# Performance work log

Hardware: AMD Instinct MI355X
Metric: run time of the kernel (lower is better)

The kernel has to match this reference:

```python
import jax, jax.numpy as jnp
import numpy as np

THR = 0.6
EPS = 1e-12


def _mlp(x, w1, b1, w2, b2):
    # Linear -> ReLU -> (Dropout eval = identity) -> Linear
    return jax.nn.relu(x @ w1 + b1) @ w2 + b2


def setup_inputs() -> dict:
    B, H, D = 16384, 1024, 300
    key = jax.random.key(0)
    ks = jax.random.split(key, 32)
    s = 0.02
    inp = {
        'brics': jax.random.normal(ks[0], (B, H), jnp.float32),
        'function_group': jax.random.normal(ks[1], (B, H), jnp.float32),
        'pharmacophore': jax.random.normal(ks[2], (B, H), jnp.float32),
        # fingerprint encoders (brics / function_group / pharmacophore)
        'bw1': jax.random.normal(ks[3], (H, D), jnp.float32) * s,
        'bb1': jnp.zeros((D,), jnp.float32),
        'bw2': jax.random.normal(ks[4], (D, H), jnp.float32) * s,
        'bb2': jnp.zeros((H,), jnp.float32),
        'fw1': jax.random.normal(ks[5], (H, D), jnp.float32) * s,
        'fb1': jnp.zeros((D,), jnp.float32),
        'fw2': jax.random.normal(ks[6], (D, H), jnp.float32) * s,
        'fb2': jnp.zeros((H,), jnp.float32),
        'pw1': jax.random.normal(ks[7], (H, D), jnp.float32) * s,
        'pb1': jnp.zeros((D,), jnp.float32),
        'pw2': jax.random.normal(ks[8], (D, H), jnp.float32) * s,
        'pb2': jnp.zeros((H,), jnp.float32),
        # weight generator: Linear(3H, 3)
        'wg_W': jax.random.normal(ks[9], (3 * H, 3), jnp.float32) * s,
        'wg_b': jnp.zeros((3,), jnp.float32),
        # enhancement layer: Linear(H, H) + sigmoid
        'enh_W': jax.random.normal(ks[10], (H, H), jnp.float32) * s,
        'enh_b': jnp.zeros((H,), jnp.float32),
        # fusion layer: Linear(2H, H)
        'fus_W': jax.random.normal(ks[11], (2 * H, H), jnp.float32) * s,
        'fus_b': jnp.zeros((H,), jnp.float32),
    }
    return inp


def reference(brics, function_group, pharmacophore,
              bw1, bb1, bw2, bb2,
              fw1, fb1, fw2, fb2,
              pw1, pb1, pw2, pb2,
              wg_W, wg_b, enh_W, enh_b, fus_W, fus_b):
    B, H = brics.shape
    eb = _mlp(brics, bw1, bb1, bw2, bb2)            # [B,H]
    ef = _mlp(function_group, fw1, fb1, fw2, fb2)   # [B,H]
    ep = _mlp(pharmacophore, pw1, pb1, pw2, pb2)    # [B,H]

    E = jnp.stack([eb, ef, ep], axis=1)             # [B,3,H]
    En = E / jnp.maximum(jnp.linalg.norm(E, axis=-1, keepdims=True), EPS)

    # three unordered pairs (0,1),(0,2),(1,2); softmax-weighted sum is
    # permutation invariant, so the original python sort is a no-op.
    ii = jnp.array([0, 0, 1])
    jj = jnp.array([1, 2, 2])
    Ei, Ej = E[:, ii], E[:, jj]                     # [B,3,H]
    Eni, Enj = En[:, ii], En[:, jj]
    sim = jnp.sum(Eni * Enj, axis=-1)               # [B,3] cosine sims
    keep = sim > THR                                # pairs above threshold

    elem_mask = (Eni * Enj > THR).astype(E.dtype)   # [B,3,H]
    cf = 0.5 * (Ei + Ej) * elem_mask                # candidate common feats

    w = jax.nn.softmax(jnp.where(keep, sim, -1e9), axis=-1)  # [B,3]
    wsum = jnp.einsum('bp,bph->bh', w, cf)
    mean_fp = jnp.mean(E, axis=1)
    any_kept = jnp.any(keep, axis=-1, keepdims=True)
    common = jnp.where(any_kept, wsum, mean_fp)     # [B,H]

    all_cat = jnp.concatenate([eb, ef, ep], axis=1)          # [B,3H]
    fp_w = jax.nn.softmax(all_cat @ wg_W + wg_b, axis=1)     # [B,3]
    weighted_fp_sum = jnp.einsum('bk,bkh->bh', fp_w, E)

    enh = jax.nn.sigmoid(common @ enh_W + enh_b)
    enhanced_common = common * enh

    fused = jnp.concatenate([weighted_fp_sum, enhanced_common], axis=1) @ fus_W + fus_b
    return fused
```

## Files before the change

kernel.cpp:

```cpp
#include <hip/hip_runtime.h>
#include <stdint.h>


typedef __attribute__((ext_vector_type(8))) __bf16 bf16x8;
typedef __attribute__((ext_vector_type(8))) short short8;
typedef __attribute__((ext_vector_type(4))) float floatx4;

__device__ __forceinline__ uint16_t f2bf(float f) {
  union { float f; uint32_t u; } v; v.f = f;
  uint32_t r = v.u + 0x7fffu + ((v.u >> 16) & 1u);
  return (uint16_t)(r >> 16);
}
__device__ __forceinline__ float bf2f(uint16_t h) {
  union { uint32_t u; float f; } v; v.u = ((uint32_t)h) << 16;
  return v.f;
}
__device__ __forceinline__ void gload16(const void* g, void* l) {
  __builtin_amdgcn_global_load_lds(
      (const __attribute__((address_space(1))) void*)g,
      (__attribute__((address_space(3))) void*)l, 16, 0, 0);
}

__global__ void cfe_cvt3_kernel(const float* __restrict__ s0,
                                const float* __restrict__ s1,
                                const float* __restrict__ s2,
                                uint16_t* __restrict__ dst) {
  const float* s = (blockIdx.y == 0) ? s0 : ((blockIdx.y == 1) ? s1 : s2);
  long i = (long)blockIdx.x * 256 + threadIdx.x;
  float4 v = ((const float4*)s)[i];
  ushort4 o;
  o.x = f2bf(v.x); o.y = f2bf(v.y); o.z = f2bf(v.z); o.w = f2bf(v.w);
  ((ushort4*)dst)[(long)blockIdx.y * (16384L * 1024 / 4) + i] = o;
}

__global__ void cfe_transpose_cvt_kernel(const float* __restrict__ src,
                                         uint16_t* __restrict__ dst,
                                         int K, int N, int Kpad, int Npad) {
  __shared__ float tile[32][33];
  const int tx = threadIdx.x & 31;
  const int ty = threadIdx.x >> 5;
  const int k0 = blockIdx.x * 32;
  const int n0 = blockIdx.y * 32;
#pragma unroll
  for (int i = 0; i < 4; i++) {
    int k = k0 + ty + 8 * i;
    int n = n0 + tx;
    tile[ty + 8 * i][tx] = (k < K && n < N) ? src[(long)k * N + n] : 0.f;
  }
  __syncthreads();
#pragma unroll
  for (int i = 0; i < 4; i++) {
    int n = n0 + ty + 8 * i;
    int k = k0 + tx;
    if (n < Npad && k < Kpad) dst[(long)n * Kpad + k] = f2bf(tile[tx][ty + 8 * i]);
  }
}

template <int MODE>
__global__ void cfe_gemm128(const uint16_t* __restrict__ A, long sAz, int lda,
                            const uint16_t* __restrict__ Bt, long sBz, int ldb,
                            void* __restrict__ C, long sCz, int ldc, int colofs,
                            const float* __restrict__ bias0,
                            const float* __restrict__ bias1,
                            const float* __restrict__ bias2, int biasN,
                            const uint16_t* __restrict__ common, int K) {
  const int z = blockIdx.z;
  A += (long)z * sAz;
  Bt += (long)z * sBz;
  const float* bias = (z == 0) ? bias0 : ((z == 1) ? bias1 : bias2);

  const int tid = threadIdx.x;
  const int wave = tid >> 6;
  const int lane = tid & 63;
  const int wm = wave >> 1;
  const int wn = wave & 1;
  const long bm = (long)blockIdx.y * 128;
  const long bn = (long)blockIdx.x * 128;

  __shared__ __attribute__((aligned(16))) uint16_t As[128 * 32];
  __shared__ __attribute__((aligned(16))) uint16_t Bs[128 * 32];

  floatx4 acc[4][4];
#pragma unroll
  for (int i = 0; i < 4; i++)
#pragma unroll
    for (int j = 0; j < 4; j++) acc[i][j] = (floatx4){0.f, 0.f, 0.f, 0.f};

  const int lrow = lane >> 2;
  const int lcol = (lane & 3) * 8;
  const uint16_t* Ap = A + (bm + wave * 32 + lrow) * (long)lda + lcol;
  const uint16_t* Bp = Bt + (bn + wave * 32 + lrow) * (long)ldb + lcol;
  uint16_t* AsW0 = &As[(wave * 32) * 32];
  uint16_t* AsW1 = &As[(wave * 32 + 16) * 32];
  uint16_t* BsW0 = &Bs[(wave * 32) * 32];
  uint16_t* BsW1 = &Bs[(wave * 32 + 16) * 32];

  const int fr = lane & 15;
  const int fq = lane >> 4;
  const uint16_t* ArBase = &As[(wm * 64 + fr) * 32 + fq * 8];
  const uint16_t* BrBase = &Bs[(wn * 64 + fr) * 32 + fq * 8];

  for (int k0 = 0; k0 < K; k0 += 32) {
    gload16(Ap + k0, AsW0);
    gload16(Ap + 16 * (long)lda + k0, AsW1);
    gload16(Bp + k0, BsW0);
    gload16(Bp + 16 * (long)ldb + k0, BsW1);
    __syncthreads();

    short8 a[4], b[4];
#pragma unroll
    for (int mi = 0; mi < 4; mi++) a[mi] = *(const short8*)(ArBase + mi * 16 * 32);
#pragma unroll
    for (int ni = 0; ni < 4; ni++) b[ni] = *(const short8*)(BrBase + ni * 16 * 32);
#pragma unroll
    for (int mi = 0; mi < 4; mi++)
#pragma unroll
      for (int ni = 0; ni < 4; ni++)
        acc[mi][ni] = __builtin_amdgcn_mfma_f32_16x16x32_bf16(
            __builtin_bit_cast(bf16x8, a[mi]), __builtin_bit_cast(bf16x8, b[ni]),
            acc[mi][ni], 0, 0, 0);
    __syncthreads();
  }

#pragma unroll
  for (int mi = 0; mi < 4; mi++) {
    long row = bm + wm * 64 + mi * 16 + fq * 4;
#pragma unroll
    for (int ni = 0; ni < 4; ni++) {
      long col = bn + wn * 64 + ni * 16 + fr;
      float bv = (col < biasN) ? bias[col] : 0.f;
#pragma unroll
      for (int r = 0; r < 4; r++) {
        float v = acc[mi][ni][r] + bv;
        long idx = (row + r) * (long)ldc + colofs + col;
        if constexpr (MODE == 0) {
          ((uint16_t*)C)[(long)z * sCz + idx] = f2bf(fmaxf(v, 0.f));
        } else if constexpr (MODE == 1) {
          ((uint16_t*)C)[(long)z * sCz + idx] = f2bf(v);
        } else if constexpr (MODE == 2) {
          float c = bf2f(common[(row + r) * 1024 + col]);
          float s = 1.f / (1.f + __expf(-v));
          ((uint16_t*)C)[idx] = f2bf(c * s);
        } else {
          ((float*)C)[idx] = v;
        }
      }
    }
  }
}

__global__ void cfe_pointwise_kernel(const uint16_t* __restrict__ E,
                                     const float* __restrict__ wgW,
                                     const float* __restrict__ wgb,
                                     uint16_t* __restrict__ commonb,
                                     uint16_t* __restrict__ fusedA) {
  const int row = blockIdx.x;
  const int tid = threadIdx.x;
  const long ES = 16384L * 1024;
  const long base = (long)row * 1024 + tid * 4;

  ushort4 u0 = *(const ushort4*)(E + base);
  ushort4 u1 = *(const ushort4*)(E + ES + base);
  ushort4 u2 = *(const ushort4*)(E + 2 * ES + base);
  float eb[4] = {bf2f(u0.x), bf2f(u0.y), bf2f(u0.z), bf2f(u0.w)};
  float ef[4] = {bf2f(u1.x), bf2f(u1.y), bf2f(u1.z), bf2f(u1.w)};
  float ep[4] = {bf2f(u2.x), bf2f(u2.y), bf2f(u2.z), bf2f(u2.w)};

  float vals[9];
#pragma unroll
  for (int i = 0; i < 9; i++) vals[i] = 0.f;
#pragma unroll
  for (int j = 0; j < 4; j++) {
    int h = tid * 4 + j;
    vals[0] += eb[j] * eb[j];
    vals[1] += ef[j] * ef[j];
    vals[2] += ep[j] * ep[j];
    vals[3] += eb[j] * ef[j];
    vals[4] += eb[j] * ep[j];
    vals[5] += ef[j] * ep[j];
#pragma unroll
    for (int c = 0; c < 3; c++)
      vals[6 + c] += eb[j] * wgW[(long)h * 3 + c] +
                     ef[j] * wgW[(long)(1024 + h) * 3 + c] +
                     ep[j] * wgW[(long)(2048 + h) * 3 + c];
  }

#pragma unroll
  for (int i = 0; i < 9; i++) {
    float v = vals[i];
    for (int off = 32; off; off >>= 1) v += __shfl_down(v, off);
    vals[i] = v;
  }
  __shared__ float red[4][9];
  if ((tid & 63) == 0) {
#pragma unroll
    for (int i = 0; i < 9; i++) red[tid >> 6][i] = vals[i];
  }
  __syncthreads();
  float tot[9];
#pragma unroll
  for (int i = 0; i < 9; i++)
    tot[i] = red[0][i] + red[1][i] + red[2][i] + red[3][i];

  const float EPSF = 1e-12f;
  float nb = fmaxf(sqrtf(tot[0]), EPSF);
  float nf = fmaxf(sqrtf(tot[1]), EPSF);
  float np_ = fmaxf(sqrtf(tot[2]), EPSF);
  float s01 = tot[3] / (nb * nf);
  float s02 = tot[4] / (nb * np_);
  float s12 = tot[5] / (nf * np_);
  bool k01 = s01 > 0.6f, k02 = s02 > 0.6f, k12 = s12 > 0.6f;
  bool any = k01 | k02 | k12;
  float z0 = k01 ? s01 : -1e9f;
  float z1 = k02 ? s02 : -1e9f;
  float z2 = k12 ? s12 : -1e9f;
  float zm = fmaxf(z0, fmaxf(z1, z2));
  float w0 = __expf(z0 - zm), w1 = __expf(z1 - zm), w2 = __expf(z2 - zm);
  float wsum = w0 + w1 + w2;
  w0 /= wsum; w1 /= wsum; w2 /= wsum;

  float g0 = tot[6] + wgb[0], g1 = tot[7] + wgb[1], g2 = tot[8] + wgb[2];
  float gm = fmaxf(g0, fmaxf(g1, g2));
  float f0 = __expf(g0 - gm), f1 = __expf(g1 - gm), f2 = __expf(g2 - gm);
  float fs = f0 + f1 + f2;
  f0 /= fs; f1 /= fs; f2 /= fs;

  float inb = 1.f / nb, inf_ = 1.f / nf, inp = 1.f / np_;
  ushort4 co, wf;
  uint16_t cov[4], wfv[4];
#pragma unroll
  for (int j = 0; j < 4; j++) {
    float b = eb[j], f = ef[j], p = ep[j];
    float nbv = b * inb, nfv = f * inf_, npv = p * inp;
    float c01 = (nbv * nfv > 0.6f) ? 0.5f * (b + f) : 0.f;
    float c02 = (nbv * npv > 0.6f) ? 0.5f * (b + p) : 0.f;
    float c12 = (nfv * npv > 0.6f) ? 0.5f * (f + p) : 0.f;
    float ws = w0 * c01 + w1 * c02 + w2 * c12;
    float cm = any ? ws : (b + f + p) * (1.f / 3.f);
    float wfs = f0 * b + f1 * f + f2 * p;
    cov[j] = f2bf(cm);
    wfv[j] = f2bf(wfs);
  }
  co.x = cov[0]; co.y = cov[1]; co.z = cov[2]; co.w = cov[3];
  wf.x = wfv[0]; wf.y = wfv[1]; wf.z = wfv[2]; wf.w = wfv[3];
  *(ushort4*)(commonb + base) = co;
  *(ushort4*)(fusedA + (long)row * 2048 + tid * 4) = wf;
}

extern "C" void kernel_launch(void* const* d_in, const int* in_sizes, int n_in,
                              void* d_out, int out_size, void* d_ws, size_t ws_size,
                              hipStream_t stream) {
  (void)in_sizes; (void)n_in; (void)out_size; (void)ws_size;
  const float* brics = (const float*)d_in[0];
  const float* fg    = (const float*)d_in[1];
  const float* ph    = (const float*)d_in[2];
  const float* bw1 = (const float*)d_in[3];  const float* bb1 = (const float*)d_in[4];
  const float* bw2 = (const float*)d_in[5];  const float* bb2 = (const float*)d_in[6];
  const float* fw1 = (const float*)d_in[7];  const float* fb1 = (const float*)d_in[8];
  const float* fw2 = (const float*)d_in[9];  const float* fb2 = (const float*)d_in[10];
  const float* pw1 = (const float*)d_in[11]; const float* pb1 = (const float*)d_in[12];
  const float* pw2 = (const float*)d_in[13]; const float* pb2 = (const float*)d_in[14];
  const float* wgW = (const float*)d_in[15]; const float* wgb = (const float*)d_in[16];
  const float* enhW = (const float*)d_in[17]; const float* enhb = (const float*)d_in[18];
  const float* fusW = (const float*)d_in[19]; const float* fusb = (const float*)d_in[20];
  float* out = (float*)d_out;

  uint16_t* XB   = (uint16_t*)d_ws;
  uint16_t* EB   = XB;
  uint16_t* FA   = XB + 3L * 16384 * 1024;
  uint16_t* W1T  = FA + 16384L * 2048;
  uint16_t* W2T  = W1T + 3L * 384 * 1024;
  uint16_t* ENHT = W2T + 3L * 1024 * 320;
  uint16_t* FUST = ENHT + 1024L * 1024;
  uint16_t* YB   = (uint16_t*)d_out;
  uint16_t* COM  = (uint16_t*)d_out;

  cfe_cvt3_kernel<<<dim3(16384, 3), 256, 0, stream>>>(brics, fg, ph, XB);

  cfe_transpose_cvt_kernel<<<dim3(32, 12), 256, 0, stream>>>(bw1, W1T + 0L * 384 * 1024, 1024, 300, 1024, 384);
  cfe_transpose_cvt_kernel<<<dim3(32, 12), 256, 0, stream>>>(fw1, W1T + 1L * 384 * 1024, 1024, 300, 1024, 384);
  cfe_transpose_cvt_kernel<<<dim3(32, 12), 256, 0, stream>>>(pw1, W1T + 2L * 384 * 1024, 1024, 300, 1024, 384);
  cfe_transpose_cvt_kernel<<<dim3(10, 32), 256, 0, stream>>>(bw2, W2T + 0L * 1024 * 320, 300, 1024, 320, 1024);
  cfe_transpose_cvt_kernel<<<dim3(10, 32), 256, 0, stream>>>(fw2, W2T + 1L * 1024 * 320, 300, 1024, 320, 1024);
  cfe_transpose_cvt_kernel<<<dim3(10, 32), 256, 0, stream>>>(pw2, W2T + 2L * 1024 * 320, 300, 1024, 320, 1024);
  cfe_transpose_cvt_kernel<<<dim3(32, 32), 256, 0, stream>>>(enhW, ENHT, 1024, 1024, 1024, 1024);
  cfe_transpose_cvt_kernel<<<dim3(64, 32), 256, 0, stream>>>(fusW, FUST, 2048, 1024, 2048, 1024);

  cfe_gemm128<0><<<dim3(3, 128, 3), 256, 0, stream>>>(
      XB, 16384L * 1024, 1024, W1T, 384L * 1024, 1024,
      YB, 16384L * 384, 384, 0, bb1, fb1, pb1, 300, nullptr, 1024);

  cfe_gemm128<1><<<dim3(8, 128, 3), 256, 0, stream>>>(
      YB, 16384L * 384, 384, W2T, 1024L * 320, 320,
      EB, 16384L * 1024, 1024, 0, bb2, fb2, pb2, 1024, nullptr, 320);

  cfe_pointwise_kernel<<<16384, 256, 0, stream>>>(EB, wgW, wgb, COM, FA);

  cfe_gemm128<2><<<dim3(8, 128, 1), 256, 0, stream>>>(
      COM, 0, 1024, ENHT, 0, 1024,
      FA, 0, 2048, 1024, enhb, enhb, enhb, 1024, COM, 1024);

  cfe_gemm128<3><<<dim3(8, 128, 1), 256, 0, stream>>>(
      FA, 0, 2048, FUST, 0, 2048,
      out, 0, 1024, 0, fusb, fusb, fusb, 1024, nullptr, 2048);
}
```

Measured before the change: 625.8 us.

## Fuse fp32-to-bf16 input conversion into first GEMM and remap block order

Removes the separate conversion kernel that turned the three fp32 input matrices into bf16. The first GEMM now reads fp32 directly, converts to bf16 in registers and stores into LDS, which avoids writing and re-reading a 96MB intermediate. Block indices are remapped with an 8-way interleave, meant to improve cache locality across concurrently running blocks. The eight weight-transpose launches are merged into four batched launches. The trade-off is that A loads in the first GEMM become synchronous register loads instead of async global-to-LDS copies, with extra conversion ALU inside the K loop.

Result: faster. 568.8 us (-9.1%).

```diff
diff --git a/kernel.cpp b/kernel.cpp
--- a/kernel.cpp
+++ b/kernel.cpp
@@ -21,21 +21,13 @@
       (__attribute__((address_space(3))) void*)l, 16, 0, 0);
 }
 
-__global__ void cfe_cvt3_kernel(const float* __restrict__ s0,
-                                const float* __restrict__ s1,
-                                const float* __restrict__ s2,
-                                uint16_t* __restrict__ dst) {
-  const float* s = (blockIdx.y == 0) ? s0 : ((blockIdx.y == 1) ? s1 : s2);
-  long i = (long)blockIdx.x * 256 + threadIdx.x;
-  float4 v = ((const float4*)s)[i];
-  ushort4 o;
-  o.x = f2bf(v.x); o.y = f2bf(v.y); o.z = f2bf(v.z); o.w = f2bf(v.w);
-  ((ushort4*)dst)[(long)blockIdx.y * (16384L * 1024 / 4) + i] = o;
-}
-
-__global__ void cfe_transpose_cvt_kernel(const float* __restrict__ src,
-                                         uint16_t* __restrict__ dst,
-                                         int K, int N, int Kpad, int Npad) {
+__global__ void cfe_transpose3_cvt_kernel(const float* __restrict__ s0,
+                                          const float* __restrict__ s1,
+                                          const float* __restrict__ s2,
+                                          uint16_t* __restrict__ dst, long dstStride,
+                                          int K, int N, int Kpad, int Npad) {
+  const float* src = (blockIdx.z == 0) ? s0 : ((blockIdx.z == 1) ? s1 : s2);
+  uint16_t* d = dst + (long)blockIdx.z * dstStride;
   __shared__ float tile[32][33];
   const int tx = threadIdx.x & 31;
   const int ty = threadIdx.x >> 5;
@@ -52,12 +44,13 @@
   for (int i = 0; i < 4; i++) {
     int n = n0 + ty + 8 * i;
     int k = k0 + tx;
-    if (n < Npad && k < Kpad) dst[(long)n * Kpad + k] = f2bf(tile[tx][ty + 8 * i]);
-  }
-}
-
-template <int MODE>
-__global__ void cfe_gemm128(const uint16_t* __restrict__ A, long sAz, int lda,
+    if (n < Npad && k < Kpad) d[(long)n * Kpad + k] = f2bf(tile[tx][ty + 8 * i]);
+  }
+}
+
+template <int MODE, int AF32>
+__global__ void cfe_gemm128(const void* __restrict__ A0, const void* __restrict__ A1,
+                            const void* __restrict__ A2, int lda,
                             const uint16_t* __restrict__ Bt, long sBz, int ldb,
                             void* __restrict__ C, long sCz, int ldc, int colofs,
                             const float* __restrict__ bias0,
@@ -65,17 +58,22 @@
                             const float* __restrict__ bias2, int biasN,
                             const uint16_t* __restrict__ common, int K) {
   const int z = blockIdx.z;
-  A += (long)z * sAz;
+  const void* Av = (z == 0) ? A0 : ((z == 1) ? A1 : A2);
   Bt += (long)z * sBz;
   const float* bias = (z == 0) ? bias0 : ((z == 1) ? bias1 : bias2);
+
+  const int gx = gridDim.x;
+  const int lin = blockIdx.y * gx + blockIdx.x;
+  const int P = (gx * gridDim.y) >> 3;
+  const int v = (lin & 7) * P + (lin >> 3);
+  const long bm = (long)(v / gx) * 128;
+  const long bn = (long)(v % gx) * 128;
 
   const int tid = threadIdx.x;
   const int wave = tid >> 6;
   const int lane = tid & 63;
   const int wm = wave >> 1;
   const int wn = wave & 1;
-  const long bm = (long)blockIdx.y * 128;
-  const long bn = (long)blockIdx.x * 128;
 
   __shared__ __attribute__((aligned(16))) uint16_t As[128 * 32];
   __shared__ __attribute__((aligned(16))) uint16_t Bs[128 * 32];
@@ -88,12 +86,22 @@
 
   const int lrow = lane >> 2;
   const int lcol = (lane & 3) * 8;
-  const uint16_t* Ap = A + (bm + wave * 32 + lrow) * (long)lda + lcol;
   const uint16_t* Bp = Bt + (bn + wave * 32 + lrow) * (long)ldb + lcol;
+  uint16_t* BsW0 = &Bs[(wave * 32) * 32];
+  uint16_t* BsW1 = &Bs[(wave * 32 + 16) * 32];
+  const uint16_t* Ap = nullptr;
   uint16_t* AsW0 = &As[(wave * 32) * 32];
   uint16_t* AsW1 = &As[(wave * 32 + 16) * 32];
-  uint16_t* BsW0 = &Bs[(wave * 32) * 32];
-  uint16_t* BsW1 = &Bs[(wave * 32 + 16) * 32];
+  const float* ApF0 = nullptr;
+  const float* ApF1 = nullptr;
+  short8* AsF0 = (short8*)&As[(wave * 32 + lrow) * 32 + lcol];
+  short8* AsF1 = (short8*)&As[(wave * 32 + 16 + lrow) * 32 + lcol];
+  if constexpr (AF32) {
+    ApF0 = (const float*)Av + (bm + wave * 32 + lrow) * (long)lda + lcol;
+    ApF1 = ApF0 + 16 * (long)lda;
+  } else {
+    Ap = (const uint16_t*)Av + (bm + wave * 32 + lrow) * (long)lda + lcol;
+  }
 
   const int fr = lane & 15;
   const int fq = lane >> 4;
@@ -101,10 +109,26 @@
   const uint16_t* BrBase = &Bs[(wn * 64 + fr) * 32 + fq * 8];
 
   for (int k0 = 0; k0 < K; k0 += 32) {
-    gload16(Ap + k0, AsW0);
-    gload16(Ap + 16 * (long)lda + k0, AsW1);
-    gload16(Bp + k0, BsW0);
-    gload16(Bp + 16 * (long)ldb + k0, BsW1);
+    if constexpr (AF32) {
+      float4 f0 = *(const float4*)(ApF0 + k0);
+      float4 f1 = *(const float4*)(ApF0 + k0 + 4);
+      float4 f2 = *(const float4*)(ApF1 + k0);
+      float4 f3 = *(const float4*)(ApF1 + k0 + 4);
+      gload16(Bp + k0, BsW0);
+      gload16(Bp + 16 * (long)ldb + k0, BsW1);
+      union { uint16_t u[8]; short8 s; } p0, p1;
+      p0.u[0] = f2bf(f0.x); p0.u[1] = f2bf(f0.y); p0.u[2] = f2bf(f0.z); p0.u[3] = f2bf(f0.w);
+      p0.u[4] = f2bf(f1.x); p0.u[5] = f2bf(f1.y); p0.u[6] = f2bf(f1.z); p0.u[7] = f2bf(f1.w);
+      p1.u[0] = f2bf(f2.x); p1.u[1] = f2bf(f2.y); p1.u[2] = f2bf(f2.z); p1.u[3] = f2bf(f2.w);
+      p1.u[4] = f2bf(f3.x); p1.u[5] = f2bf(f3.y); p1.u[6] = f2bf(f3.z); p1.u[7] = f2bf(f3.w);
+      *AsF0 = p0.s;
+      *AsF1 = p1.s;
+    } else {
+      gload16(Ap + k0, AsW0);
+      gload16(Ap + 16 * (long)lda + k0, AsW1);
+      gload16(Bp + k0, BsW0);
+      gload16(Bp + 16 * (long)ldb + k0, BsW1);
+    }
     __syncthreads();
 
     short8 a[4], b[4];
@@ -131,18 +155,18 @@
       float bv = (col < biasN) ? bias[col] : 0.f;
 #pragma unroll
       for (int r = 0; r < 4; r++) {
-        float v = acc[mi][ni][r] + bv;
+        float vv = acc[mi][ni][r] + bv;
         long idx = (row + r) * (long)ldc + colofs + col;
         if constexpr (MODE == 0) {
-          ((uint16_t*)C)[(long)z * sCz + idx] = f2bf(fmaxf(v, 0.f));
+          ((uint16_t*)C)[(long)z * sCz + idx] = f2bf(fmaxf(vv, 0.f));
         } else if constexpr (MODE == 1) {
-          ((uint16_t*)C)[(long)z * sCz + idx] = f2bf(v);
+          ((uint16_t*)C)[(long)z * sCz + idx] = f2bf(vv);
         } else if constexpr (MODE == 2) {
           float c = bf2f(common[(row + r) * 1024 + col]);
-          float s = 1.f / (1.f + __expf(-v));
+          float s = 1.f / (1.f + __expf(-vv));
           ((uint16_t*)C)[idx] = f2bf(c * s);
         } else {
-          ((float*)C)[idx] = v;
+          ((float*)C)[idx] = vv;
         }
       }
     }
@@ -265,9 +289,8 @@
   const float* fusW = (const float*)d_in[19]; const float* fusb = (const float*)d_in[20];
   float* out = (float*)d_out;
 
-  uint16_t* XB   = (uint16_t*)d_ws;
-  uint16_t* EB   = XB;
-  uint16_t* FA   = XB + 3L * 16384 * 1024;
+  uint16_t* EB   = (uint16_t*)d_ws;
+  uint16_t* FA   = EB + 3L * 16384 * 1024;
   uint16_t* W1T  = FA + 16384L * 2048;
   uint16_t* W2T  = W1T + 3L * 384 * 1024;
   uint16_t* ENHT = W2T + 3L * 1024 * 320;
@@ -275,32 +298,30 @@
   uint16_t* YB   = (uint16_t*)d_out;
   uint16_t* COM  = (uint16_t*)d_out;
 
-  cfe_cvt3_kernel<<<dim3(16384, 3), 256, 0, stream>>>(brics, fg, ph, XB);
-
-  cfe_transpose_cvt_kernel<<<dim3(32, 12), 256, 0, stream>>>(bw1, W1T + 0L * 384 * 1024, 1024, 300, 1024, 384);
-  cfe_transpose_cvt_kernel<<<dim3(32, 12), 256, 0, stream>>>(fw1, W1T + 1L * 384 * 1024, 1024, 300, 1024, 384);
-  cfe_transpose_cvt_kernel<<<dim3(32, 12), 256, 0, stream>>>(pw1, W1T + 2L * 384 * 1024, 1024, 300, 1024, 384);
-  cfe_transpose_cvt_kernel<<<dim3(10, 32), 256, 0, stream>>>(bw2, W2T + 0L * 1024 * 320, 300, 1024, 320, 1024);
-  cfe_transpose_cvt_kernel<<<dim3(10, 32), 256, 0, stream>>>(fw2, W2T + 1L * 1024 * 320, 300, 1024, 320, 1024);
-  cfe_transpose_cvt_kernel<<<dim3(10, 32), 256, 0, stream>>>(pw2, W2T + 2L * 1024 * 320, 300, 1024, 320, 1024);
-  cfe_transpose_cvt_kernel<<<dim3(32, 32), 256, 0, stream>>>(enhW, ENHT, 1024, 1024, 1024, 1024);
-  cfe_transpose_cvt_kernel<<<dim3(64, 32), 256, 0, stream>>>(fusW, FUST, 2048, 1024, 2048, 1024);
-
-  cfe_gemm128<0><<<dim3(3, 128, 3), 256, 0, stream>>>(
-      XB, 16384L * 1024, 1024, W1T, 384L * 1024, 1024,
+  cfe_transpose3_cvt_kernel<<<dim3(32, 12, 3), 256, 0, stream>>>(
+      bw1, fw1, pw1, W1T, 384L * 1024, 1024, 300, 1024, 384);
+  cfe_transpose3_cvt_kernel<<<dim3(10, 32, 3), 256, 0, stream>>>(
+      bw2, fw2, pw2, W2T, 1024L * 320, 300, 1024, 320, 1024);
+  cfe_transpose3_cvt_kernel<<<dim3(32, 32, 1), 256, 0, stream>>>(
+      enhW, enhW, enhW, ENHT, 0, 1024, 1024, 1024, 1024);
+  cfe_transpose3_cvt_kernel<<<dim3(64, 32, 1), 256, 0, stream>>>(
+      fusW, fusW, fusW, FUST, 0, 2048, 1024, 2048, 1024);
+
+  cfe_gemm128<0, 1><<<dim3(3, 128, 3), 256, 0, stream>>>(
+      brics, fg, ph, 1024, W1T, 384L * 1024, 1024,
       YB, 16384L * 384, 384, 0, bb1, fb1, pb1, 300, nullptr, 1024);
 
-  cfe_gemm128<1><<<dim3(8, 128, 3), 256, 0, stream>>>(
-      YB, 16384L * 384, 384, W2T, 1024L * 320, 320,
+  cfe_gemm128<1, 0><<<dim3(8, 128, 3), 256, 0, stream>>>(
+      YB, YB + 16384L * 384, YB + 2 * 16384L * 384, 384, W2T, 1024L * 320, 320,
       EB, 16384L * 1024, 1024, 0, bb2, fb2, pb2, 1024, nullptr, 320);
 
   cfe_pointwise_kernel<<<16384, 256, 0, stream>>>(EB, wgW, wgb, COM, FA);
 
-  cfe_gemm128<2><<<dim3(8, 128, 1), 256, 0, stream>>>(
-      COM, 0, 1024, ENHT, 0, 1024,
+  cfe_gemm128<2, 0><<<dim3(8, 128, 1), 256, 0, stream>>>(
+      COM, COM, COM, 1024, ENHT, 0, 1024,
       FA, 0, 2048, 1024, enhb, enhb, enhb, 1024, COM, 1024);
 
-  cfe_gemm128<3><<<dim3(8, 128, 1), 256, 0, stream>>>(
-      FA, 0, 2048, FUST, 0, 2048,
+  cfe_gemm128<3, 0><<<dim3(8, 128, 1), 256, 0, stream>>>(
+      FA, FA, FA, 2048, FUST, 0, 2048,
       out, 0, 1024, 0, fusb, fusb, fusb, 1024, nullptr, 2048);
 }
```
